# Performance work log

Hardware: AMD Instinct MI355X
Metric: run time of the kernel (lower is better)

## Reference

```python
import jax, jax.numpy as jnp
import numpy as np

N = 32768   # nodes
E = 32768   # edges
ND, ED, GD = 12, 5, 11
H = 64
T = 4
STEPS = 3


def setup_inputs() -> dict:
    key = jax.random.key(0)
    ks = jax.random.split(key, 24)
    s = 0.05
    p = lambda k, sh: (jax.random.normal(k, sh) * s).astype(jnp.float32)
    return dict(
        x=jax.random.normal(ks[0], (N, ND), jnp.float32),
        edge_index=jax.random.randint(ks[1], (2, E), 0, N, jnp.int64),
        edge_attr=jax.random.uniform(ks[2], (E, ED), jnp.float32),
        u=jax.random.normal(ks[3], (1, GD), jnp.float32),
        Wp=p(ks[4], (H, ND + GD)), bp=p(ks[5], (H,)),
        We1=p(ks[6], (H, ED)), be1=p(ks[7], (H,)),
        We2=p(ks[8], (H * H, H)), be2=p(ks[9], (H * H,)),
        root=p(ks[10], (H, H)), conv_b=p(ks[11], (H,)),
        Wih=p(ks[12], (3 * H, H)), bih=p(ks[13], (3 * H,)),
        Whh=p(ks[14], (3 * H, H)), bhh=p(ks[15], (3 * H,)),
        Wd1=p(ks[16], (H, 2 * H + ED)), bd1=p(ks[17], (H,)),
        Wd2=p(ks[18], (H // 2, H)), bd2=p(ks[19], (H // 2,)),
        Wd3=p(ks[20], (T, H // 2)), bd3=p(ks[21], (T,)),
    )


def _forward(x, edge_index, edge_attr, u,
             Wp, bp, We1, be1, We2, be2, root, conv_b,
             Wih, bih, Whh, bhh, Wd1, bd1, Wd2, bd2, Wd3, bd3):
    n = x.shape[0]
    e = edge_attr.shape[0]
    src, dst = edge_index[0], edge_index[1]

    # input projection with broadcast global features (batch=None path)
    u_node = jnp.broadcast_to(u, (n, u.shape[-1]))
    h = jnp.tanh(jnp.concatenate([x, u_node], axis=-1) @ Wp.T + bp)

    # edge MLP -> per-edge (H,H) weight matrices; edge_attr is loop-invariant
    ew = jax.nn.relu(edge_attr @ We1.T + be1) @ We2.T + be2   # (E, H*H)
    ew = ew.reshape(e, H, H)                                   # (E, H, H)

    # mean-aggregation denominators (clamped to 1 like scatter-mean)
    counts = jnp.clip(jax.ops.segment_sum(jnp.ones((e,), h.dtype), dst, num_segments=n), 1.0)

    for _ in range(STEPS):
        # NNConv: gather src features, per-edge matmul, scatter-mean into dst
        msg = jnp.einsum('eh,eho->eo', h[src], ew)             # (E, H)
        agg = jax.ops.segment_sum(msg, dst, num_segments=n) / counts[:, None]
        m = jax.nn.relu(agg + h @ root + conv_b)               # dropout off (eval)
        # GRUCell (torch gate order: r, z, n)
        gi = m @ Wih.T + bih
        gh = h @ Whh.T + bhh
        r = jax.nn.sigmoid(gi[:, :H] + gh[:, :H])
        z = jax.nn.sigmoid(gi[:, H:2 * H] + gh[:, H:2 * H])
        ng = jnp.tanh(gi[:, 2 * H:] + r * gh[:, 2 * H:])
        h = (1.0 - z) * ng + z * h

    # per-edge decoder
    e_in = jnp.concatenate([h[src], h[dst], edge_attr], axis=-1)
    d = jax.nn.relu(e_in @ Wd1.T + bd1)
    d = jax.nn.relu(d @ Wd2.T + bd2)
    return d @ Wd3.T + bd3                                     # (E, T)


def reference(x, edge_index, edge_attr, u,
              Wp, bp, We1, be1, We2, be2, root, conv_b,
              Wih, bih, Whh, bhh, Wd1, bd1, Wd2, bd2, Wd3, bd3):
    return _forward(x, edge_index, edge_attr, u,
                    Wp, bp, We1, be1, We2, be2, root, conv_b,
                    Wih, bih, Whh, bhh, Wd1, bd1, Wd2, bd2, Wd3, bd3)
```

## Files before the change

kernel.cpp:

```cpp
#include <hip/hip_runtime.h>
#include <hip/hip_bf16.h>
#include <stdint.h>


#define N_NODES 32768
#define N_EDGES 32768
#define STEPS 3

typedef __attribute__((ext_vector_type(8))) short short8;
typedef __attribute__((ext_vector_type(4))) float float4v;

__device__ __forceinline__ float bf2f(unsigned short u) {
    union { unsigned int i; float f; } v; v.i = ((unsigned int)u) << 16; return v.f;
}
__device__ __forceinline__ unsigned short f2bf(float f) {
    union { float f; unsigned int i; } v; v.f = f;
    unsigned int x = v.i;
    return (unsigned short)((x + 0x7fffu + ((x >> 16) & 1u)) >> 16);
}

__device__ __forceinline__ void gload_lds16(const void* g, void* l) {
    __builtin_amdgcn_global_load_lds(
        (__attribute__((address_space(1))) void*)g,
        (__attribute__((address_space(3))) void*)l, 16, 0, 0);
}

__global__ __launch_bounds__(256) void k_setup(
    const float* __restrict__ root, const float* __restrict__ Wih,
    const float* __restrict__ Whh,
    const float* __restrict__ We2, const float* __restrict__ be2,
    const float* __restrict__ Wd1, const float* __restrict__ bd1,
    const float* __restrict__ Wd2,
    const float* __restrict__ x, const float* __restrict__ u,
    const float* __restrict__ Wp, const float* __restrict__ bp,
    const float* __restrict__ ea, const float* __restrict__ We1,
    const float* __restrict__ be1,
    unsigned short* __restrict__ rootTf, unsigned short* __restrict__ wcombf,
    unsigned short* __restrict__ w2tf,
    unsigned short* __restrict__ wd1f, unsigned short* __restrict__ wd2f,
    unsigned short* __restrict__ hb,
    unsigned short* __restrict__ hidT, float* __restrict__ cnts)
{
    int b = blockIdx.x, tid = threadIdx.x;
    if (b < 144) {
        int i = b * 256 + tid;
        if (i < 4096) {
            int j = i & 7, lane = (i >> 3) & 63, g = i >> 9;
            int kb = g >> 2, nf = g & 3;
            int o = nf * 16 + (lane & 15);
            int k = kb * 32 + (lane >> 4) * 8 + j;
            rootTf[i] = f2bf(root[k * 64 + o]);
        } else if (i < 4096 + 32768) {
            int t = i - 4096;
            int j = t & 7, lane = (t >> 3) & 63, g = t >> 9;
            int kb = g >> 4, nf = g & 15;
            int cp = nf * 16 + (lane & 15);
            int k = kb * 32 + (lane >> 4) * 8 + j;
            float v;
            if (cp < 128)      v = (k < 64) ? Wih[cp * 64 + k] : Whh[cp * 64 + (k - 64)];
            else if (cp < 192) v = (k < 64) ? Wih[cp * 64 + k] : 0.f;
            else               v = (k < 64) ? 0.f : Whh[(cp - 64) * 64 + (k - 64)];
            wcombf[t] = f2bf(v);
        }
    } else if (b < 1184) {
        int t = (b - 144) * 256 + tid;
        if (t < 65 * 4096) {
            int kk = t >> 12, r = t & 4095;
            int j = r & 7, lane = (r >> 3) & 63, g = r >> 9;
            int half = g >> 2, nf = g & 3;
            int o = nf * 16 + (lane & 15);
            int hh = half * 32 + (lane >> 4) * 8 + j;
            float v = (kk < 64) ? We2[((size_t)(hh * 64 + o)) * 64 + kk]
                                : be2[(size_t)hh * 64 + o];
            w2tf[t] = f2bf(v);
        }
    } else if (b < 1232) {
        int i = (b - 1184) * 256 + tid;
        if (i < 10240) {
            int j = i & 7, lane = (i >> 3) & 63, g = i >> 9;
            int kb = g >> 2, nf = g & 3;
            int o = nf * 16 + (lane & 15);
            int k = kb * 32 + (lane >> 4) * 8 + j;
            float v = (k < 133) ? Wd1[(size_t)o * 133 + k] : (k == 133 ? bd1[o] : 0.f);
            wd1f[i] = f2bf(v);
        } else if (i < 10240 + 2048) {
            int t = i - 10240;
            int j = t & 7, lane = (t >> 3) & 63, g = t >> 9;
            int kb = g >> 1, nf = g & 1;
            int o = nf * 16 + (lane & 15);
            int k = kb * 32 + (lane >> 4) * 8 + j;
            wd2f[t] = f2bf(Wd2[(size_t)o * 64 + k]);
        }
    } else if (b < 9424) {
        int idx = (b - 1232) * 256 + tid;
        int n = idx >> 6, j = idx & 63;
        const float* wr = Wp + j * 23;
        const float* xr = x + (size_t)n * 12;
        float s = bp[j];
#pragma unroll
        for (int i = 0; i < 12; i++) s += xr[i] * wr[i];
#pragma unroll
        for (int i = 0; i < 11; i++) s += u[i] * wr[12 + i];
        hb[idx] = f2bf(tanhf(s));
    } else if (b < 17616) {
        int idx = (b - 9424) * 256 + tid;
        int el = idx & 63, j = (idx >> 6) & 63, eb = idx >> 12;
        int e = eb * 64 + el;
        float s = be1[j];
#pragma unroll
        for (int i = 0; i < 5; i++) s += ea[(size_t)e * 5 + i] * We1[j * 5 + i];
        hidT[(size_t)j * N_EDGES + e] = f2bf(s > 0.f ? s : 0.f);
    } else {
        int idx = (b - 17616) * 1024 + tid * 4;
        if (idx < 32768) {
            float4v z = {0.f, 0.f, 0.f, 0.f};
            *(float4v*)(cnts + idx) = z;
        }
    }
}

__global__ __launch_bounds__(256) void k_counts(
    const int* __restrict__ ei, float* __restrict__ counts)
{
    int i = blockIdx.x * 256 + threadIdx.x;
    if (i < N_EDGES) atomicAdd(&counts[ei[N_EDGES + i]], 1.0f);
}

__global__ __launch_bounds__(1024) void k_scan(
    const float* __restrict__ cnts, int* __restrict__ off, int* __restrict__ woff)
{
    __shared__ int part[1024];
    int t = threadIdx.x;
    int loc[32];
    int s = 0;
#pragma unroll
    for (int i = 0; i < 32; i++) { loc[i] = s; s += (int)cnts[t * 32 + i]; }
    part[t] = s;
    __syncthreads();
    for (int d = 1; d < 1024; d <<= 1) {
        int y = (t >= d) ? part[t - d] : 0;
        __syncthreads();
        part[t] += y;
        __syncthreads();
    }
    int pre = (t == 0) ? 0 : part[t - 1];
#pragma unroll
    for (int i = 0; i < 32; i++) {
        off[t * 32 + i] = pre + loc[i];
        woff[t * 32 + i] = pre + loc[i];
    }
    if (t == 1023) off[32768] = part[1023];
}

__global__ __launch_bounds__(256) void k_scatter(
    const int* __restrict__ ei, int* __restrict__ woff, int* __restrict__ eorder)
{
    int e = blockIdx.x * 256 + threadIdx.x;
    if (e < N_EDGES) {
        int d = ei[N_EDGES + e];
        int slot = atomicAdd(&woff[d], 1);
        eorder[slot] = e;
    }
}

__global__ __launch_bounds__(512, 2) void k_msg_fused(
    const unsigned short* __restrict__ hidT,
    const unsigned short* __restrict__ hb,
    const unsigned short* __restrict__ w2tf,
    const int* __restrict__ ei,
    float* __restrict__ msgbuf)
{
    __shared__ __attribute__((aligned(16))) unsigned char smem[98304];
    unsigned short* stg = (unsigned short*)smem;
    unsigned short* hvl = (unsigned short*)(smem + 65536);
    float* red = (float*)smem;

    int tid = threadIdx.x, w = tid >> 6, lane = tid & 63;
    int l15 = lane & 15, quad = lane >> 4;
    int kg = w & 3, nfh = w >> 2;
    int ebase = blockIdx.x * 128;
    int n_w = 16 + (kg == 3 ? 1 : 0);

    unsigned short* hvp = hvl + w * 2048;
#pragma unroll
    for (int r2 = 0; r2 < 16; r2++) {
        unsigned int v = *((const unsigned int*)(hidT + (size_t)(kg * 16 + r2) * N_EDGES + ebase) + lane);
        *((unsigned int*)hvp + r2 * 64 + lane) = v;
    }
    short8 afr[8][2];
#pragma unroll
    for (int t = 0; t < 8; t++) {
        int src = ei[ebase + t * 16 + l15];
#pragma unroll
        for (int hh = 0; hh < 2; hh++)
            afr[t][hh] = *(const short8*)(hb + (size_t)src * 64 + hh * 32 + quad * 8);
    }

    unsigned short* wbuf = stg + w * 4096;
    auto stage = [&](int r, int db) {
        const unsigned short* g = w2tf + (size_t)(kg * 16 + r) * 4096;
        unsigned short* d = wbuf + db * 2048;
#pragma unroll
        for (int c = 0; c < 4; c++) {
            int hh = c >> 1, j = c & 1;
            gload_lds16(g + (hh * 4 + nfh * 2 + j) * 512 + lane * 8, d + c * 512);
        }
    };

    stage(0, 0);
    stage(1, 1);
    asm volatile("s_waitcnt lgkmcnt(0)" ::: "memory");

    float4v acc[8][2] = {};
    for (int r = 0; r < n_w; r++) {
        int db = r & 1;
        if (r < n_w - 1) { asm volatile("s_waitcnt vmcnt(4)" ::: "memory"); }
        else             { asm volatile("s_waitcnt vmcnt(0)" ::: "memory"); }

        bool bias = (r == 16);
        short8 bfr[2][2];
        const unsigned short* bb = wbuf + db * 2048;
#pragma unroll
        for (int hh = 0; hh < 2; hh++)
#pragma unroll
            for (int j = 0; j < 2; j++)
                bfr[hh][j] = *(const short8*)(bb + (hh * 2 + j) * 512 + lane * 8);

        unsigned long long hu[8] = {};
        if (!bias) {
#pragma unroll
            for (int t = 0; t < 8; t++)
                hu[t] = *(const unsigned long long*)(hvp + r * 128 + t * 16 + quad * 4);
        }

        asm volatile("s_waitcnt lgkmcnt(0)" ::: "memory");
        if (r + 2 < n_w) stage(r + 2, db);

#pragma unroll
        for (int t = 0; t < 8; t++) {
            float4v z = {0.f, 0.f, 0.f, 0.f};
            float4v T0 = __builtin_amdgcn_mfma_f32_16x16x32_bf16(afr[t][0], bfr[0][0], z, 0, 0, 0);
            T0 = __builtin_amdgcn_mfma_f32_16x16x32_bf16(afr[t][1], bfr[1][0], T0, 0, 0, 0);
            float4v T1 = __builtin_amdgcn_mfma_f32_16x16x32_bf16(afr[t][0], bfr[0][1], z, 0, 0, 0);
            T1 = __builtin_amdgcn_mfma_f32_16x16x32_bf16(afr[t][1], bfr[1][1], T1, 0, 0, 0);
#pragma unroll
            for (int rr = 0; rr < 4; rr++) {
                float hvv = bias ? 1.0f : bf2f((unsigned short)(hu[t] >> (16 * rr)));
                acc[t][0][rr] += hvv * T0[rr];
                acc[t][1][rr] += hvv * T1[rr];
            }
        }
    }

    int row_r = tid >> 2, cq = tid & 3;
#pragma unroll
    for (int nf2 = 0; nf2 < 2; nf2++) {
        __syncthreads();
#pragma unroll
        for (int t = 0; t < 8; t++)
#pragma unroll
            for (int rr = 0; rr < 4; rr++)
                red[kg * 4352 + (t * 16 + quad * 4 + rr) * 34 + nfh * 16 + l15] = acc[t][nf2][rr];
        __syncthreads();
        float s[8];
#pragma unroll
        for (int i = 0; i < 8; i++) s[i] = 0.f;
#pragma unroll
        for (int g2 = 0; g2 < 4; g2++) {
            const float* rp = red + g2 * 4352 + row_r * 34 + cq * 8;
#pragma unroll
            for (int i = 0; i < 8; i++) s[i] += rp[i];
        }
        int c34 = cq * 8;
        int gcol = ((c34 >> 4) * 2 + nf2) * 16 + (c34 & 15);
        float* op = msgbuf + (size_t)(ebase + row_r) * 64 + gcol;
        float4v v0 = { s[0], s[1], s[2], s[3] };
        float4v v1 = { s[4], s[5], s[6], s[7] };
        *(float4v*)(op) = v0;
        *(float4v*)(op + 4) = v1;
    }
}

__global__ __launch_bounds__(256) void k_node(
    const unsigned short* __restrict__ hb_in,
    const unsigned short* __restrict__ rootTf,
    const unsigned short* __restrict__ wcombf,
    const float* __restrict__ msgbuf, const int* __restrict__ off,
    const int* __restrict__ eorder,
    const float* __restrict__ counts,
    const float* __restrict__ conv_b,
    const float* __restrict__ bih, const float* __restrict__ bhh,
    unsigned short* __restrict__ hb_out)
{
    __shared__ unsigned short m_lds[64 * 72];
    __shared__ float aggl[64 * 68];
    int tid = threadIdx.x, w = tid >> 6, lane = tid & 63;
    int l15 = lane & 15, quad = lane >> 4;
    int node0 = blockIdx.x * 64;
    int row0 = w * 16;

    {
        int nl = tid >> 2, cg = tid & 3;
        int nn = node0 + nl;
        int s0 = off[nn], s1 = off[nn + 1];
        float acc[16] = {};
        for (int sl = s0; sl < s1; sl++) {
            int e = eorder[sl];
            const float* mr = msgbuf + (size_t)e * 64 + cg * 16;
#pragma unroll
            for (int q = 0; q < 4; q++) {
                float4v v = *(const float4v*)(mr + 4 * q);
#pragma unroll
                for (int j = 0; j < 4; j++) acc[4 * q + j] += v[j];
            }
        }
#pragma unroll
        for (int k = 0; k < 16; k++) aggl[nl * 68 + cg * 16 + k] = acc[k];
    }
    __syncthreads();

    float4v acc1[4] = {};
    {
        short8 a1[2];
#pragma unroll
        for (int kb = 0; kb < 2; kb++)
            a1[kb] = *(const short8*)(hb_in + (size_t)(node0 + row0 + l15) * 64 + kb * 32 + quad * 8);
#pragma unroll
        for (int kb = 0; kb < 2; kb++)
#pragma unroll
            for (int nf = 0; nf < 4; nf++) {
                short8 b = *(const short8*)(rootTf + (size_t)((kb * 4 + nf) * 64 + lane) * 8);
                acc1[nf] = __builtin_amdgcn_mfma_f32_16x16x32_bf16(a1[kb], b, acc1[nf], 0, 0, 0);
            }
    }
#pragma unroll
    for (int rr = 0; rr < 4; rr++) {
        int nl = row0 + quad * 4 + rr;
        float cnt = counts[node0 + nl]; if (cnt < 1.f) cnt = 1.f;
        float rcp = 1.f / cnt;
#pragma unroll
        for (int nf = 0; nf < 4; nf++) {
            int c = nf * 16 + l15;
            float av = aggl[nl * 68 + c];
            float mv = av * rcp + acc1[nf][rr] + conv_b[c];
            m_lds[nl * 72 + c] = f2bf(mv > 0.f ? mv : 0.f);
        }
    }
    __syncthreads();

    float4v acc2[16] = {};
#pragma unroll
    for (int kb = 0; kb < 4; kb++) {
        short8 a2;
        if (kb < 2)
            a2 = *(const short8*)(m_lds + (row0 + l15) * 72 + kb * 32 + quad * 8);
        else
            a2 = *(const short8*)(hb_in + (size_t)(node0 + row0 + l15) * 64 + (kb - 2) * 32 + quad * 8);
#pragma unroll
        for (int nf = 0; nf < 16; nf++) {
            short8 b = *(const short8*)(wcombf + (size_t)((kb * 16 + nf) * 64 + lane) * 8);
            acc2[nf] = __builtin_amdgcn_mfma_f32_16x16x32_bf16(a2, b, acc2[nf], 0, 0, 0);
        }
    }

#pragma unroll
    for (int nf0 = 0; nf0 < 4; nf0++) {
        int c = nf0 * 16 + l15;
        float br = bih[c] + bhh[c];
        float bz = bih[64 + c] + bhh[64 + c];
        float bni = bih[128 + c], bnh = bhh[128 + c];
#pragma unroll
        for (int rr = 0; rr < 4; rr++) {
            int node = node0 + row0 + quad * 4 + rr;
            float gr = 1.f / (1.f + __expf(-(acc2[nf0][rr] + br)));
            float gz = 1.f / (1.f + __expf(-(acc2[nf0 + 4][rr] + bz)));
            float ng = tanhf(acc2[nf0 + 8][rr] + bni + gr * (acc2[nf0 + 12][rr] + bnh));
            float ho = bf2f(hb_in[(size_t)node * 64 + c]);
            float hn = (1.f - gz) * ng + gz * ho;
            hb_out[(size_t)node * 64 + c] = f2bf(hn);
        }
    }
}

__global__ __launch_bounds__(256) void k_decoder(
    const unsigned short* __restrict__ hb, const int* __restrict__ ei,
    const float* __restrict__ ea,
    const unsigned short* __restrict__ wd1f, const unsigned short* __restrict__ wd2f,
    const float* __restrict__ bd2,
    const float* __restrict__ Wd3, const float* __restrict__ bd3,
    float* __restrict__ out)
{
    __shared__ unsigned short d1f[4][1024];
    __shared__ float d2s[4][16 * 33];
    int tid = threadIdx.x, w = tid >> 6, lane = tid & 63;
    int l15 = lane & 15, quad = lane >> 4;
    int ebase = blockIdx.x * 64 + w * 16;
    int e = ebase + l15;
    int src = ei[e], dst = ei[N_EDGES + e];

    short8 a[5];
#pragma unroll
    for (int kb = 0; kb < 2; kb++) {
        a[kb]     = *(const short8*)(hb + (size_t)src * 64 + kb * 32 + quad * 8);
        a[2 + kb] = *(const short8*)(hb + (size_t)dst * 64 + kb * 32 + quad * 8);
    }
    {
        union { short8 v; unsigned short u[8]; } tea;
#pragma unroll
        for (int j = 0; j < 8; j++) {
            float vv = 0.f;
            if (quad == 0) vv = (j < 5) ? ea[(size_t)e * 5 + j] : (j == 5 ? 1.f : 0.f);
            tea.u[j] = f2bf(vv);
        }
        a[4] = tea.v;
    }

    float4v acc1[4] = {};
#pragma unroll
    for (int kb = 0; kb < 5; kb++)
#pragma unroll
        for (int nf = 0; nf < 4; nf++) {
            short8 b = *(const short8*)(wd1f + (size_t)((kb * 4 + nf) * 64 + lane) * 8);
            acc1[nf] = __builtin_amdgcn_mfma_f32_16x16x32_bf16(a[kb], b, acc1[nf], 0, 0, 0);
        }
#pragma unroll
    for (int nf = 0; nf < 4; nf++) {
        int kbp = nf >> 1;
        int lanep_hi = ((nf & 1) * 2 + (l15 >> 3)) * 16;
        int jp = l15 & 7;
#pragma unroll
        for (int r = 0; r < 4; r++) {
            float v = acc1[nf][r];
            d1f[w][kbp * 512 + (lanep_hi + quad * 4 + r) * 8 + jp] = f2bf(v > 0.f ? v : 0.f);
        }
    }
    float4v acc2[2] = {};
#pragma unroll
    for (int kb = 0; kb < 2; kb++) {
        short8 a2 = *(const short8*)(&d1f[w][kb * 512 + lane * 8]);
#pragma unroll
        for (int nf = 0; nf < 2; nf++) {
            short8 b = *(const short8*)(wd2f + (size_t)((kb * 2 + nf) * 64 + lane) * 8);
            acc2[nf] = __builtin_amdgcn_mfma_f32_16x16x32_bf16(a2, b, acc2[nf], 0, 0, 0);
        }
    }
#pragma unroll
    for (int nf = 0; nf < 2; nf++) {
        int c = nf * 16 + l15;
        float bias = bd2[c];
#pragma unroll
        for (int r = 0; r < 4; r++) {
            float v = acc2[nf][r] + bias;
            d2s[w][(quad * 4 + r) * 33 + c] = v > 0.f ? v : 0.f;
        }
    }
    {
        int e_l = lane >> 2, t = lane & 3;
        float s = bd3[t];
        const float* w3 = Wd3 + t * 32;
        const float* dr = &d2s[w][e_l * 33];
#pragma unroll
        for (int k = 0; k < 32; k++) s += w3[k] * dr[k];
        out[(size_t)(ebase + e_l) * 4 + t] = s;
    }
}

extern "C" void kernel_launch(void* const* d_in, const int* in_sizes, int n_in,
                              void* d_out, int out_size, void* d_ws, size_t ws_size,
                              hipStream_t stream)
{
    const float* x      = (const float*)d_in[0];
    const int*   ei     = (const int*)d_in[1];
    const float* ea     = (const float*)d_in[2];
    const float* u      = (const float*)d_in[3];
    const float* Wp     = (const float*)d_in[4];
    const float* bp     = (const float*)d_in[5];
    const float* We1    = (const float*)d_in[6];
    const float* be1    = (const float*)d_in[7];
    const float* We2    = (const float*)d_in[8];
    const float* be2    = (const float*)d_in[9];
    const float* root   = (const float*)d_in[10];
    const float* conv_b = (const float*)d_in[11];
    const float* Wih    = (const float*)d_in[12];
    const float* bih    = (const float*)d_in[13];
    const float* Whh    = (const float*)d_in[14];
    const float* bhh    = (const float*)d_in[15];
    const float* Wd1    = (const float*)d_in[16];
    const float* bd1    = (const float*)d_in[17];
    const float* Wd2    = (const float*)d_in[18];
    const float* bd2    = (const float*)d_in[19];
    const float* Wd3    = (const float*)d_in[20];
    const float* bd3    = (const float*)d_in[21];
    float* out = (float*)d_out;

    char* ws = (char*)d_ws;
    size_t off_b = 0;
    auto take = [&](size_t bytes) -> char* {
        char* p = ws + off_b; off_b = (off_b + bytes + 255) & ~(size_t)255; return p;
    };
    unsigned short* hb     = (unsigned short*)take((size_t)N_NODES * 64 * 2);
    unsigned short* hidT   = (unsigned short*)take((size_t)N_EDGES * 64 * 2);
    float*          msgbuf = (float*)take((size_t)N_EDGES * 64 * 4);
    float*          cnts   = (float*)take((size_t)N_NODES * 4);
    int*            off    = (int*)take((size_t)(N_NODES + 1) * 4);
    int*            woff   = (int*)take((size_t)N_NODES * 4);
    int*            eorder = (int*)take((size_t)N_EDGES * 4);
    unsigned short* w2tf   = (unsigned short*)take((size_t)66 * 4096 * 2);
    unsigned short* rootTf = (unsigned short*)take((size_t)4096 * 2);
    unsigned short* wcombf = (unsigned short*)take((size_t)32768 * 2);
    unsigned short* wd1f   = (unsigned short*)take((size_t)10240 * 2);
    unsigned short* wd2f   = (unsigned short*)take((size_t)2048 * 2);
    (void)ws_size;

    k_setup<<<17648, 256, 0, stream>>>(root, Wih, Whh, We2, be2, Wd1, bd1, Wd2,
                                       x, u, Wp, bp, ea, We1, be1,
                                       rootTf, wcombf, w2tf, wd1f, wd2f,
                                       hb, hidT, cnts);
    k_counts<<<128, 256, 0, stream>>>(ei, cnts);
    k_scan<<<1, 1024, 0, stream>>>(cnts, off, woff);
    k_scatter<<<128, 256, 0, stream>>>(ei, woff, eorder);

    for (int s = 0; s < STEPS; s++) {
        k_msg_fused<<<N_EDGES / 128, 512, 0, stream>>>(hidT, hb, w2tf, ei, msgbuf);
        k_node<<<N_NODES / 64, 256, 0, stream>>>(hb, rootTf, wcombf, msgbuf, off,
                                                 eorder, cnts, conv_b, bih, bhh, hb);
    }
    k_decoder<<<N_EDGES / 64, 256, 0, stream>>>(hb, ei, ea, wd1f, wd2f, bd2,
                                                Wd3, bd3, out);
}
```

Baseline: 261.9 us.

## Fuse message, node-update and decoder kernels into one persistent grid-barrier kernel

Replaces the per-step message and node kernel launches and the final decoder launch with a single persistent kernel of 256 blocks. A software grid barrier (atomic counter plus generation flag) separates the message, aggregation/GRU and decoder phases. Each block now covers 128 edges and 128 nodes, and reuses one shared-memory buffer across phases. This removes the launch gaps and tail effects between the seven kernels. The risks are spin-barrier overhead, and a deadlock if all 256 blocks cannot be resident at once.

```diff
diff --git a/kernel.cpp b/kernel.cpp
--- a/kernel.cpp
+++ b/kernel.cpp
@@ -6,6 +6,7 @@
 #define N_NODES 32768
 #define N_EDGES 32768
 #define STEPS 3
+#define NBLK 256
 
 typedef __attribute__((ext_vector_type(8))) short short8;
 typedef __attribute__((ext_vector_type(4))) float float4v;
@@ -23,6 +24,24 @@
     __builtin_amdgcn_global_load_lds(
         (__attribute__((address_space(1))) void*)g,
         (__attribute__((address_space(3))) void*)l, 16, 0, 0);
+}
+
+__device__ __forceinline__ void grid_barrier(unsigned int* bar) {
+    __syncthreads();
+    if (threadIdx.x == 0) {
+        __threadfence();
+        unsigned g = __hip_atomic_load(&bar[1], __ATOMIC_RELAXED, __HIP_MEMORY_SCOPE_AGENT);
+        unsigned v = __hip_atomic_fetch_add(&bar[0], 1u, __ATOMIC_ACQ_REL, __HIP_MEMORY_SCOPE_AGENT);
+        if (v == (unsigned)(NBLK - 1)) {
+            __hip_atomic_store(&bar[0], 0u, __ATOMIC_RELAXED, __HIP_MEMORY_SCOPE_AGENT);
+            __hip_atomic_store(&bar[1], g + 1u, __ATOMIC_RELEASE, __HIP_MEMORY_SCOPE_AGENT);
+        } else {
+            while (__hip_atomic_load(&bar[1], __ATOMIC_ACQUIRE, __HIP_MEMORY_SCOPE_AGENT) == g)
+                __builtin_amdgcn_s_sleep(8);
+        }
+        __threadfence();
+    }
+    __syncthreads();
 }
 
 __global__ __launch_bounds__(256) void k_setup(
@@ -127,10 +146,12 @@
 }
 
 __global__ __launch_bounds__(1024) void k_scan(
-    const float* __restrict__ cnts, int* __restrict__ off, int* __restrict__ woff)
+    const float* __restrict__ cnts, int* __restrict__ off, int* __restrict__ woff,
+    unsigned int* __restrict__ bar)
 {
     __shared__ int part[1024];
     int t = threadIdx.x;
+    if (t == 0) { bar[0] = 0u; bar[1] = 0u; }
     int loc[32];
     int s = 0;
 #pragma unroll
@@ -163,22 +184,39 @@
     }
 }
 
-__global__ __launch_bounds__(512, 2) void k_msg_fused(
+__global__ __launch_bounds__(512, 2) void k_mega(
     const unsigned short* __restrict__ hidT,
-    const unsigned short* __restrict__ hb,
+    unsigned short* __restrict__ hb,
     const unsigned short* __restrict__ w2tf,
     const int* __restrict__ ei,
-    float* __restrict__ msgbuf)
+    float* __restrict__ msgbuf,
+    const unsigned short* __restrict__ rootTf,
+    const unsigned short* __restrict__ wcombf,
+    const int* __restrict__ off, const int* __restrict__ eorder,
+    const float* __restrict__ cnts, const float* __restrict__ conv_b,
+    const float* __restrict__ bih, const float* __restrict__ bhh,
+    const float* __restrict__ ea,
+    const unsigned short* __restrict__ wd1f, const unsigned short* __restrict__ wd2f,
+    const float* __restrict__ bd2,
+    const float* __restrict__ Wd3, const float* __restrict__ bd3,
+    float* __restrict__ out,
+    unsigned int* __restrict__ bar)
 {
-    __shared__ __attribute__((aligned(16))) unsigned char smem[98304];
-    unsigned short* stg = (unsigned short*)smem;
-    unsigned short* hvl = (unsigned short*)(smem + 65536);
-    float* red = (float*)smem;
+    __shared__ __attribute__((aligned(16))) unsigned char smem[102400];
+    unsigned short* stg   = (unsigned short*)smem;
+    unsigned short* hvl   = (unsigned short*)(smem + 69632);
+    float*          red   = (float*)smem;
+    unsigned short* m_lds = (unsigned short*)smem;
+    float*          aggl  = (float*)(smem + 18432);
+    unsigned short* d1f   = (unsigned short*)smem;
+    float*          d2s   = (float*)(smem + 16384);
 
     int tid = threadIdx.x, w = tid >> 6, lane = tid & 63;
     int l15 = lane & 15, quad = lane >> 4;
+    int bid = blockIdx.x;
     int kg = w & 3, nfh = w >> 2;
-    int ebase = blockIdx.x * 128;
+    int ebase = bid * 128;
+    int node0 = bid * 128;
     int n_w = 16 + (kg == 3 ? 1 : 0);
 
     unsigned short* hvp = hvl + w * 2048;
@@ -186,14 +224,6 @@
     for (int r2 = 0; r2 < 16; r2++) {
         unsigned int v = *((const unsigned int*)(hidT + (size_t)(kg * 16 + r2) * N_EDGES + ebase) + lane);
         *((unsigned int*)hvp + r2 * 64 + lane) = v;
-    }
-    short8 afr[8][2];
-#pragma unroll
-    for (int t = 0; t < 8; t++) {
-        int src = ei[ebase + t * 16 + l15];
-#pragma unroll
-        for (int hh = 0; hh < 2; hh++)
-            afr[t][hh] = *(const short8*)(hb + (size_t)src * 64 + hh * 32 + quad * 8);
     }
 
     unsigned short* wbuf = stg + w * 4096;
@@ -207,261 +237,246 @@
         }
     };
 
-    stage(0, 0);
-    stage(1, 1);
-    asm volatile("s_waitcnt lgkmcnt(0)" ::: "memory");
-
-    float4v acc[8][2] = {};
-    for (int r = 0; r < n_w; r++) {
-        int db = r & 1;
-        if (r < n_w - 1) { asm volatile("s_waitcnt vmcnt(4)" ::: "memory"); }
-        else             { asm volatile("s_waitcnt vmcnt(0)" ::: "memory"); }
-
-        bool bias = (r == 16);
-        short8 bfr[2][2];
-        const unsigned short* bb = wbuf + db * 2048;
-#pragma unroll
-        for (int hh = 0; hh < 2; hh++)
-#pragma unroll
-            for (int j = 0; j < 2; j++)
-                bfr[hh][j] = *(const short8*)(bb + (hh * 2 + j) * 512 + lane * 8);
-
-        unsigned long long hu[8] = {};
-        if (!bias) {
+    for (int step = 0; step < STEPS; step++) {
+        short8 afr[8][2];
+#pragma unroll
+        for (int t = 0; t < 8; t++) {
+            int src = ei[ebase + t * 16 + l15];
+#pragma unroll
+            for (int hh = 0; hh < 2; hh++)
+                afr[t][hh] = *(const short8*)(hb + (size_t)src * 64 + hh * 32 + quad * 8);
+        }
+        stage(0, 0);
+        stage(1, 1);
+        asm volatile("s_waitcnt lgkmcnt(0)" ::: "memory");
+
+        float4v acc[8][2] = {};
+        for (int r = 0; r < n_w; r++) {
+            int db = r & 1;
+            if (r < n_w - 1) { asm volatile("s_waitcnt vmcnt(4)" ::: "memory"); }
+            else             { asm volatile("s_waitcnt vmcnt(0)" ::: "memory"); }
+
+            bool bias = (r == 16);
+            short8 bfr[2][2];
+            const unsigned short* bb = wbuf + db * 2048;
+#pragma unroll
+            for (int hh = 0; hh < 2; hh++)
+#pragma unroll
+                for (int j = 0; j < 2; j++)
+                    bfr[hh][j] = *(const short8*)(bb + (hh * 2 + j) * 512 + lane * 8);
+
+            unsigned long long hu[8] = {};
+            if (!bias) {
+#pragma unroll
+                for (int t = 0; t < 8; t++)
+                    hu[t] = *(const unsigned long long*)(hvp + r * 128 + t * 16 + quad * 4);
+            }
+
+            asm volatile("s_waitcnt lgkmcnt(0)" ::: "memory");
+            if (r + 2 < n_w) stage(r + 2, db);
+
+#pragma unroll
+            for (int t = 0; t < 8; t++) {
+                float4v z = {0.f, 0.f, 0.f, 0.f};
+                float4v T0 = __builtin_amdgcn_mfma_f32_16x16x32_bf16(afr[t][0], bfr[0][0], z, 0, 0, 0);
+                T0 = __builtin_amdgcn_mfma_f32_16x16x32_bf16(afr[t][1], bfr[1][0], T0, 0, 0, 0);
+                float4v T1 = __builtin_amdgcn_mfma_f32_16x16x32_bf16(afr[t][0], bfr[0][1], z, 0, 0, 0);
+                T1 = __builtin_amdgcn_mfma_f32_16x16x32_bf16(afr[t][1], bfr[1][1], T1, 0, 0, 0);
+#pragma unroll
+                for (int rr = 0; rr < 4; rr++) {
+                    float hvv = bias ? 1.0f : bf2f((unsigned short)(hu[t] >> (16 * rr)));
+                    acc[t][0][rr] += hvv * T0[rr];
+                    acc[t][1][rr] += hvv * T1[rr];
+                }
+            }
+        }
+
+        int row_r = tid >> 2, cq = tid & 3;
+#pragma unroll
+        for (int nf2 = 0; nf2 < 2; nf2++) {
+            __syncthreads();
 #pragma unroll
             for (int t = 0; t < 8; t++)
-                hu[t] = *(const unsigned long long*)(hvp + r * 128 + t * 16 + quad * 4);
-        }
-
-        asm volatile("s_waitcnt lgkmcnt(0)" ::: "memory");
-        if (r + 2 < n_w) stage(r + 2, db);
-
-#pragma unroll
-        for (int t = 0; t < 8; t++) {
-            float4v z = {0.f, 0.f, 0.f, 0.f};
-            float4v T0 = __builtin_amdgcn_mfma_f32_16x16x32_bf16(afr[t][0], bfr[0][0], z, 0, 0, 0);
-            T0 = __builtin_amdgcn_mfma_f32_16x16x32_bf16(afr[t][1], bfr[1][0], T0, 0, 0, 0);
-            float4v T1 = __builtin_amdgcn_mfma_f32_16x16x32_bf16(afr[t][0], bfr[0][1], z, 0, 0, 0);
-            T1 = __builtin_amdgcn_mfma_f32_16x16x32_bf16(afr[t][1], bfr[1][1], T1, 0, 0, 0);
+#pragma unroll
+                for (int rr = 0; rr < 4; rr++)
+                    red[kg * 4352 + (t * 16 + quad * 4 + rr) * 34 + nfh * 16 + l15] = acc[t][nf2][rr];
+            __syncthreads();
+            float s[8];
+#pragma unroll
+            for (int i = 0; i < 8; i++) s[i] = 0.f;
+#pragma unroll
+            for (int g2 = 0; g2 < 4; g2++) {
+                const float* rp = red + g2 * 4352 + row_r * 34 + cq * 8;
+#pragma unroll
+                for (int i = 0; i < 8; i++) s[i] += rp[i];
+            }
+            int c34 = cq * 8;
+            int gcol = ((c34 >> 4) * 2 + nf2) * 16 + (c34 & 15);
+            float* op = msgbuf + (size_t)(ebase + row_r) * 64 + gcol;
+            float4v v0 = { s[0], s[1], s[2], s[3] };
+            float4v v1 = { s[4], s[5], s[6], s[7] };
+            *(float4v*)(op) = v0;
+            *(float4v*)(op + 4) = v1;
+        }
+
+        grid_barrier(bar);
+
+        {
+            int nl = tid >> 2, cg = tid & 3;
+            int nn = node0 + nl;
+            int s0 = off[nn], s1 = off[nn + 1];
+            float accg[16] = {};
+            for (int sl = s0; sl < s1; sl++) {
+                int e = eorder[sl];
+                const float* mr = msgbuf + (size_t)e * 64 + cg * 16;
+#pragma unroll
+                for (int q = 0; q < 4; q++) {
+                    float4v v = *(const float4v*)(mr + 4 * q);
+#pragma unroll
+                    for (int j = 0; j < 4; j++) accg[4 * q + j] += v[j];
+                }
+            }
+#pragma unroll
+            for (int k = 0; k < 16; k++) aggl[nl * 68 + cg * 16 + k] = accg[k];
+        }
+        __syncthreads();
+
+        int row0 = w * 16;
+        float4v acc1[4] = {};
+        {
+            short8 a1[2];
+#pragma unroll
+            for (int kb = 0; kb < 2; kb++)
+                a1[kb] = *(const short8*)(hb + (size_t)(node0 + row0 + l15) * 64 + kb * 32 + quad * 8);
+#pragma unroll
+            for (int kb = 0; kb < 2; kb++)
+#pragma unroll
+                for (int nf = 0; nf < 4; nf++) {
+                    short8 b = *(const short8*)(rootTf + (size_t)((kb * 4 + nf) * 64 + lane) * 8);
+                    acc1[nf] = __builtin_amdgcn_mfma_f32_16x16x32_bf16(a1[kb], b, acc1[nf], 0, 0, 0);
+                }
+        }
+#pragma unroll
+        for (int rr = 0; rr < 4; rr++) {
+            int nl = row0 + quad * 4 + rr;
+            float cnt = cnts[node0 + nl]; if (cnt < 1.f) cnt = 1.f;
+            float rcp = 1.f / cnt;
+#pragma unroll
+            for (int nf = 0; nf < 4; nf++) {
+                int c = nf * 16 + l15;
+                float av = aggl[nl * 68 + c];
+                float mv = av * rcp + acc1[nf][rr] + conv_b[c];
+                m_lds[nl * 72 + c] = f2bf(mv > 0.f ? mv : 0.f);
+            }
+        }
+        __syncthreads();
+
+        float4v acc2[16] = {};
+#pragma unroll
+        for (int kb = 0; kb < 4; kb++) {
+            short8 a2;
+            if (kb < 2)
+                a2 = *(const short8*)(m_lds + (row0 + l15) * 72 + kb * 32 + quad * 8);
+            else
+                a2 = *(const short8*)(hb + (size_t)(node0 + row0 + l15) * 64 + (kb - 2) * 32 + quad * 8);
+#pragma unroll
+            for (int nf = 0; nf < 16; nf++) {
+                short8 b = *(const short8*)(wcombf + (size_t)((kb * 16 + nf) * 64 + lane) * 8);
+                acc2[nf] = __builtin_amdgcn_mfma_f32_16x16x32_bf16(a2, b, acc2[nf], 0, 0, 0);
+            }
+        }
+
+#pragma unroll
+        for (int nf0 = 0; nf0 < 4; nf0++) {
+            int c = nf0 * 16 + l15;
+            float br = bih[c] + bhh[c];
+            float bz = bih[64 + c] + bhh[64 + c];
+            float bni = bih[128 + c], bnh = bhh[128 + c];
 #pragma unroll
             for (int rr = 0; rr < 4; rr++) {
-                float hvv = bias ? 1.0f : bf2f((unsigned short)(hu[t] >> (16 * rr)));
-                acc[t][0][rr] += hvv * T0[rr];
-                acc[t][1][rr] += hvv * T1[rr];
-            }
-        }
-    }
-
-    int row_r = tid >> 2, cq = tid & 3;
-#pragma unroll
-    for (int nf2 = 0; nf2 < 2; nf2++) {
-        __syncthreads();
-#pragma unroll
-        for (int t = 0; t < 8; t++)
-#pragma unroll
-            for (int rr = 0; rr < 4; rr++)
-                red[kg * 4352 + (t * 16 + quad * 4 + rr) * 34 + nfh * 16 + l15] = acc[t][nf2][rr];
-        __syncthreads();
-        float s[8];
-#pragma unroll
-        for (int i = 0; i < 8; i++) s[i] = 0.f;
-#pragma unroll
-        for (int g2 = 0; g2 < 4; g2++) {
-            const float* rp = red + g2 * 4352 + row_r * 34 + cq * 8;
-#pragma unroll
-            for (int i = 0; i < 8; i++) s[i] += rp[i];
-        }
-        int c34 = cq * 8;
-        int gcol = ((c34 >> 4) * 2 + nf2) * 16 + (c34 & 15);
-        float* op = msgbuf + (size_t)(ebase + row_r) * 64 + gcol;
-        float4v v0 = { s[0], s[1], s[2], s[3] };
-        float4v v1 = { s[4], s[5], s[6], s[7] };
-        *(float4v*)(op) = v0;
-        *(float4v*)(op + 4) = v1;
-    }
-}
-
-__global__ __launch_bounds__(256) void k_node(
-    const unsigned short* __restrict__ hb_in,
-    const unsigned short* __restrict__ rootTf,
-    const unsigned short* __restrict__ wcombf,
-    const float* __restrict__ msgbuf, const int* __restrict__ off,
-    const int* __restrict__ eorder,
-    const float* __restrict__ counts,
-    const float* __restrict__ conv_b,
-    const float* __restrict__ bih, const float* __restrict__ bhh,
-    unsigned short* __restrict__ hb_out)
-{
-    __shared__ unsigned short m_lds[64 * 72];
-    __shared__ float aggl[64 * 68];
-    int tid = threadIdx.x, w = tid >> 6, lane = tid & 63;
-    int l15 = lane & 15, quad = lane >> 4;
-    int node0 = blockIdx.x * 64;
-    int row0 = w * 16;
+                int node = node0 + row0 + quad * 4 + rr;
+                float gr = 1.f / (1.f + __expf(-(acc2[nf0][rr] + br)));
+                float gz = 1.f / (1.f + __expf(-(acc2[nf0 + 4][rr] + bz)));
+                float ng = tanhf(acc2[nf0 + 8][rr] + bni + gr * (acc2[nf0 + 12][rr] + bnh));
+                float ho = bf2f(hb[(size_t)node * 64 + c]);
+                float hn = (1.f - gz) * ng + gz * ho;
+                hb[(size_t)node * 64 + c] = f2bf(hn);
+            }
+        }
+
+        grid_barrier(bar);
+    }
 
     {
-        int nl = tid >> 2, cg = tid & 3;
-        int nn = node0 + nl;
-        int s0 = off[nn], s1 = off[nn + 1];
-        float acc[16] = {};
-        for (int sl = s0; sl < s1; sl++) {
-            int e = eorder[sl];
-            const float* mr = msgbuf + (size_t)e * 64 + cg * 16;
-#pragma unroll
-            for (int q = 0; q < 4; q++) {
-                float4v v = *(const float4v*)(mr + 4 * q);
-#pragma unroll
-                for (int j = 0; j < 4; j++) acc[4 * q + j] += v[j];
-            }
-        }
-#pragma unroll
-        for (int k = 0; k < 16; k++) aggl[nl * 68 + cg * 16 + k] = acc[k];
-    }
-    __syncthreads();
-
-    float4v acc1[4] = {};
-    {
-        short8 a1[2];
-#pragma unroll
-        for (int kb = 0; kb < 2; kb++)
-            a1[kb] = *(const short8*)(hb_in + (size_t)(node0 + row0 + l15) * 64 + kb * 32 + quad * 8);
-#pragma unroll
-        for (int kb = 0; kb < 2; kb++)
+        int eb_d = bid * 128 + w * 16;
+        int e = eb_d + l15;
+        int src = ei[e], dst = ei[N_EDGES + e];
+
+        short8 a[5];
+#pragma unroll
+        for (int kb = 0; kb < 2; kb++) {
+            a[kb]     = *(const short8*)(hb + (size_t)src * 64 + kb * 32 + quad * 8);
+            a[2 + kb] = *(const short8*)(hb + (size_t)dst * 64 + kb * 32 + quad * 8);
+        }
+        {
+            union { short8 v; unsigned short u[8]; } tea;
+#pragma unroll
+            for (int j = 0; j < 8; j++) {
+                float vv = 0.f;
+                if (quad == 0) vv = (j < 5) ? ea[(size_t)e * 5 + j] : (j == 5 ? 1.f : 0.f);
+                tea.u[j] = f2bf(vv);
+            }
+            a[4] = tea.v;
+        }
+
+        float4v acc1[4] = {};
+#pragma unroll
+        for (int kb = 0; kb < 5; kb++)
 #pragma unroll
             for (int nf = 0; nf < 4; nf++) {
-                short8 b = *(const short8*)(rootTf + (size_t)((kb * 4 + nf) * 64 + lane) * 8);
-                acc1[nf] = __builtin_amdgcn_mfma_f32_16x16x32_bf16(a1[kb], b, acc1[nf], 0, 0, 0);
-            }
-    }
-#pragma unroll
-    for (int rr = 0; rr < 4; rr++) {
-        int nl = row0 + quad * 4 + rr;
-        float cnt = counts[node0 + nl]; if (cnt < 1.f) cnt = 1.f;
-        float rcp = 1.f / cnt;
+                short8 b = *(const short8*)(wd1f + (size_t)((kb * 4 + nf) * 64 + lane) * 8);
+                acc1[nf] = __builtin_amdgcn_mfma_f32_16x16x32_bf16(a[kb], b, acc1[nf], 0, 0, 0);
+            }
 #pragma unroll
         for (int nf = 0; nf < 4; nf++) {
+            int kbp = nf >> 1;
+            int lanep_hi = ((nf & 1) * 2 + (l15 >> 3)) * 16;
+            int jp = l15 & 7;
+#pragma unroll
+            for (int r = 0; r < 4; r++) {
+                float v = acc1[nf][r];
+                d1f[w * 1024 + kbp * 512 + (lanep_hi + quad * 4 + r) * 8 + jp] = f2bf(v > 0.f ? v : 0.f);
+            }
+        }
+        float4v acc2[2] = {};
+#pragma unroll
+        for (int kb = 0; kb < 2; kb++) {
+            short8 a2 = *(const short8*)(&d1f[w * 1024 + kb * 512 + lane * 8]);
+#pragma unroll
+            for (int nf = 0; nf < 2; nf++) {
+                short8 b = *(const short8*)(wd2f + (size_t)((kb * 2 + nf) * 64 + lane) * 8);
+                acc2[nf] = __builtin_amdgcn_mfma_f32_16x16x32_bf16(a2, b, acc2[nf], 0, 0, 0);
+            }
+        }
+#pragma unroll
+        for (int nf = 0; nf < 2; nf++) {
             int c = nf * 16 + l15;
-            float av = aggl[nl * 68 + c];
-            float mv = av * rcp + acc1[nf][rr] + conv_b[c];
-            m_lds[nl * 72 + c] = f2bf(mv > 0.f ? mv : 0.f);
-        }
-    }
-    __syncthreads();
-
-    float4v acc2[16] = {};
-#pragma unroll
-    for (int kb = 0; kb < 4; kb++) {
-        short8 a2;
-        if (kb < 2)
-            a2 = *(const short8*)(m_lds + (row0 + l15) * 72 + kb * 32 + quad * 8);
-        else
-            a2 = *(const short8*)(hb_in + (size_t)(node0 + row0 + l15) * 64 + (kb - 2) * 32 + quad * 8);
-#pragma unroll
-        for (int nf = 0; nf < 16; nf++) {
-            short8 b = *(const short8*)(wcombf + (size_t)((kb * 16 + nf) * 64 + lane) * 8);
-            acc2[nf] = __builtin_amdgcn_mfma_f32_16x16x32_bf16(a2, b, acc2[nf], 0, 0, 0);
-        }
-    }
-
-#pragma unroll
-    for (int nf0 = 0; nf0 < 4; nf0++) {
-        int c = nf0 * 16 + l15;
-        float br = bih[c] + bhh[c];
-        float bz = bih[64 + c] + bhh[64 + c];
-        float bni = bih[128 + c], bnh = bhh[128 + c];
-#pragma unroll
-        for (int rr = 0; rr < 4; rr++) {
-            int node = node0 + row0 + quad * 4 + rr;
-            float gr = 1.f / (1.f + __expf(-(acc2[nf0][rr] + br)));
-            float gz = 1.f / (1.f + __expf(-(acc2[nf0 + 4][rr] + bz)));
-            float ng = tanhf(acc2[nf0 + 8][rr] + bni + gr * (acc2[nf0 + 12][rr] + bnh));
-            float ho = bf2f(hb_in[(size_t)node * 64 + c]);
-            float hn = (1.f - gz) * ng + gz * ho;
-            hb_out[(size_t)node * 64 + c] = f2bf(hn);
-        }
-    }
-}
-
-__global__ __launch_bounds__(256) void k_decoder(
-    const unsigned short* __restrict__ hb, const int* __restrict__ ei,
-    const float* __restrict__ ea,
-    const unsigned short* __restrict__ wd1f, const unsigned short* __restrict__ wd2f,
-    const float* __restrict__ bd2,
-    const float* __restrict__ Wd3, const float* __restrict__ bd3,
-    float* __restrict__ out)
-{
-    __shared__ unsigned short d1f[4][1024];
-    __shared__ float d2s[4][16 * 33];
-    int tid = threadIdx.x, w = tid >> 6, lane = tid & 63;
-    int l15 = lane & 15, quad = lane >> 4;
-    int ebase = blockIdx.x * 64 + w * 16;
-    int e = ebase + l15;
-    int src = ei[e], dst = ei[N_EDGES + e];
-
-    short8 a[5];
-#pragma unroll
-    for (int kb = 0; kb < 2; kb++) {
-        a[kb]     = *(const short8*)(hb + (size_t)src * 64 + kb * 32 + quad * 8);
-        a[2 + kb] = *(const short8*)(hb + (size_t)dst * 64 + kb * 32 + quad * 8);
-    }
-    {
-        union { short8 v; unsigned short u[8]; } tea;
-#pragma unroll
-        for (int j = 0; j < 8; j++) {
-            float vv = 0.f;
-            if (quad == 0) vv = (j < 5) ? ea[(size_t)e * 5 + j] : (j == 5 ? 1.f : 0.f);
-            tea.u[j] = f2bf(vv);
-        }
-        a[4] = tea.v;
-    }
-
-    float4v acc1[4] = {};
-#pragma unroll
-    for (int kb = 0; kb < 5; kb++)
-#pragma unroll
-        for (int nf = 0; nf < 4; nf++) {
-            short8 b = *(const short8*)(wd1f + (size_t)((kb * 4 + nf) * 64 + lane) * 8);
-            acc1[nf] = __builtin_amdgcn_mfma_f32_16x16x32_bf16(a[kb], b, acc1[nf], 0, 0, 0);
-        }
-#pragma unroll
-    for (int nf = 0; nf < 4; nf++) {
-        int kbp = nf >> 1;
-        int lanep_hi = ((nf & 1) * 2 + (l15 >> 3)) * 16;
-        int jp = l15 & 7;
-#pragma unroll
-        for (int r = 0; r < 4; r++) {
-            float v = acc1[nf][r];
-            d1f[w][kbp * 512 + (lanep_hi + quad * 4 + r) * 8 + jp] = f2bf(v > 0.f ? v : 0.f);
-        }
-    }
-    float4v acc2[2] = {};
-#pragma unroll
-    for (int kb = 0; kb < 2; kb++) {
-        short8 a2 = *(const short8*)(&d1f[w][kb * 512 + lane * 8]);
-#pragma unroll
-        for (int nf = 0; nf < 2; nf++) {
-            short8 b = *(const short8*)(wd2f + (size_t)((kb * 2 + nf) * 64 + lane) * 8);
-            acc2[nf] = __builtin_amdgcn_mfma_f32_16x16x32_bf16(a2, b, acc2[nf], 0, 0, 0);
-        }
-    }
-#pragma unroll
-    for (int nf = 0; nf < 2; nf++) {
-        int c = nf * 16 + l15;
-        float bias = bd2[c];
-#pragma unroll
-        for (int r = 0; r < 4; r++) {
-            float v = acc2[nf][r] + bias;
-            d2s[w][(quad * 4 + r) * 33 + c] = v > 0.f ? v : 0.f;
-        }
-    }
-    {
-        int e_l = lane >> 2, t = lane & 3;
-        float s = bd3[t];
-        const float* w3 = Wd3 + t * 32;
-        const float* dr = &d2s[w][e_l * 33];
-#pragma unroll
-        for (int k = 0; k < 32; k++) s += w3[k] * dr[k];
-        out[(size_t)(ebase + e_l) * 4 + t] = s;
+            float bias = bd2[c];
+#pragma unroll
+            for (int r = 0; r < 4; r++) {
+                float v = acc2[nf][r] + bias;
+                d2s[w * 528 + (quad * 4 + r) * 33 + c] = v > 0.f ? v : 0.f;
+            }
+        }
+        {
+            int e_l = lane >> 2, t = lane & 3;
+            float s = bd3[t];
+            const float* w3 = Wd3 + t * 32;
+            const float* dr = &d2s[w * 528 + e_l * 33];
+#pragma unroll
+            for (int k = 0; k < 32; k++) s += w3[k] * dr[k];
+            out[(size_t)(eb_d + e_l) * 4 + t] = s;
+        }
     }
 }
 
@@ -505,6 +520,7 @@
     int*            off    = (int*)take((size_t)(N_NODES + 1) * 4);
     int*            woff   = (int*)take((size_t)N_NODES * 4);
     int*            eorder = (int*)take((size_t)N_EDGES * 4);
+    unsigned int*   bar    = (unsigned int*)take(256);
     unsigned short* w2tf   = (unsigned short*)take((size_t)66 * 4096 * 2);
     unsigned short* rootTf = (unsigned short*)take((size_t)4096 * 2);
     unsigned short* wcombf = (unsigned short*)take((size_t)32768 * 2);
@@ -517,14 +533,11 @@
                                        rootTf, wcombf, w2tf, wd1f, wd2f,
                                        hb, hidT, cnts);
     k_counts<<<128, 256, 0, stream>>>(ei, cnts);
-    k_scan<<<1, 1024, 0, stream>>>(cnts, off, woff);
+    k_scan<<<1, 1024, 0, stream>>>(cnts, off, woff, bar);
     k_scatter<<<128, 256, 0, stream>>>(ei, woff, eorder);
 
-    for (int s = 0; s < STEPS; s++) {
-        k_msg_fused<<<N_EDGES / 128, 512, 0, stream>>>(hidT, hb, w2tf, ei, msgbuf);
-        k_node<<<N_NODES / 64, 256, 0, stream>>>(hb, rootTf, wcombf, msgbuf, off,
-                                                 eorder, cnts, conv_b, bih, bhh, hb);
-    }
-    k_decoder<<<N_EDGES / 64, 256, 0, stream>>>(hb, ei, ea, wd1f, wd2f, bd2,
-                                                Wd3, bd3, out);
-}
+    k_mega<<<NBLK, 512, 0, stream>>>(hidT, hb, w2tf, ei, msgbuf,
+                                     rootTf, wcombf, off, eorder, cnts,
+                                     conv_b, bih, bhh, ea, wd1f, wd2f,
+                                     bd2, Wd3, bd3, out, bar);
+}
```

After: 611.4 us. +133.4%, slower.

## Fuse graph CSR build into one LDS kernel and halve msg tile per block

Applied to the files above, without the earlier changes.

Replaces the counts/scan/scatter kernels with a single 1024-thread kernel that counts in-degree with LDS atomics, scans, and fills the edge order, removing two launches and the global atomics. The fused message kernel now handles 64 edges per block instead of 128, using 72KB of LDS and fewer accumulator registers, and targets 4 blocks per CU for higher occupancy. The cost is that each block re-streams the whole edge-weight matrix for half as many edges, doubling weight traffic, and the single-block graph build runs serially on one CU.

```diff
diff --git a/kernel.cpp b/kernel.cpp
--- a/kernel.cpp
+++ b/kernel.cpp
@@ -39,7 +39,7 @@
     unsigned short* __restrict__ w2tf,
     unsigned short* __restrict__ wd1f, unsigned short* __restrict__ wd2f,
     unsigned short* __restrict__ hb,
-    unsigned short* __restrict__ hidT, float* __restrict__ cnts)
+    unsigned short* __restrict__ hidT)
 {
     int b = blockIdx.x, tid = threadIdx.x;
     if (b < 144) {
@@ -102,7 +102,7 @@
 #pragma unroll
         for (int i = 0; i < 11; i++) s += u[i] * wr[12 + i];
         hb[idx] = f2bf(tanhf(s));
-    } else if (b < 17616) {
+    } else {
         int idx = (b - 9424) * 256 + tid;
         int el = idx & 63, j = (idx >> 6) & 63, eb = idx >> 12;
         int e = eb * 64 + el;
@@ -110,31 +110,28 @@
 #pragma unroll
         for (int i = 0; i < 5; i++) s += ea[(size_t)e * 5 + i] * We1[j * 5 + i];
         hidT[(size_t)j * N_EDGES + e] = f2bf(s > 0.f ? s : 0.f);
-    } else {
-        int idx = (b - 17616) * 1024 + tid * 4;
-        if (idx < 32768) {
-            float4v z = {0.f, 0.f, 0.f, 0.f};
-            *(float4v*)(cnts + idx) = z;
-        }
-    }
-}
-
-__global__ __launch_bounds__(256) void k_counts(
-    const int* __restrict__ ei, float* __restrict__ counts)
+    }
+}
+
+__global__ __launch_bounds__(1024) void k_graph(
+    const int* __restrict__ ei, int* __restrict__ off,
+    float* __restrict__ cnts, int* __restrict__ eorder)
 {
-    int i = blockIdx.x * 256 + threadIdx.x;
-    if (i < N_EDGES) atomicAdd(&counts[ei[N_EDGES + i]], 1.0f);
-}
-
-__global__ __launch_bounds__(1024) void k_scan(
-    const float* __restrict__ cnts, int* __restrict__ off, int* __restrict__ woff)
-{
+    __shared__ int cnt[N_NODES];
     __shared__ int part[1024];
     int t = threadIdx.x;
-    int loc[32];
-    int s = 0;
-#pragma unroll
-    for (int i = 0; i < 32; i++) { loc[i] = s; s += (int)cnts[t * 32 + i]; }
+#pragma unroll
+    for (int i = 0; i < 32; i++) cnt[t + i * 1024] = 0;
+    __syncthreads();
+#pragma unroll
+    for (int i = 0; i < 32; i++) {
+        int e = t + i * 1024;
+        atomicAdd(&cnt[ei[N_EDGES + e]], 1);
+    }
+    __syncthreads();
+    int loc[32]; int s = 0;
+#pragma unroll
+    for (int i = 0; i < 32; i++) { loc[i] = s; s += cnt[t * 32 + i]; }
     part[t] = s;
     __syncthreads();
     for (int d = 1; d < 1024; d <<= 1) {
@@ -144,33 +141,36 @@
         __syncthreads();
     }
     int pre = (t == 0) ? 0 : part[t - 1];
+    int base[32];
 #pragma unroll
     for (int i = 0; i < 32; i++) {
-        off[t * 32 + i] = pre + loc[i];
-        woff[t * 32 + i] = pre + loc[i];
-    }
-    if (t == 1023) off[32768] = part[1023];
-}
-
-__global__ __launch_bounds__(256) void k_scatter(
-    const int* __restrict__ ei, int* __restrict__ woff, int* __restrict__ eorder)
-{
-    int e = blockIdx.x * 256 + threadIdx.x;
-    if (e < N_EDGES) {
+        int n = t * 32 + i;
+        base[i] = pre + loc[i];
+        off[n] = base[i];
+        cnts[n] = (float)cnt[n];
+    }
+    if (t == 1023) off[N_NODES] = N_EDGES;
+    __syncthreads();
+#pragma unroll
+    for (int i = 0; i < 32; i++) cnt[t * 32 + i] = base[i];
+    __syncthreads();
+#pragma unroll
+    for (int i = 0; i < 32; i++) {
+        int e = t + i * 1024;
         int d = ei[N_EDGES + e];
-        int slot = atomicAdd(&woff[d], 1);
+        int slot = atomicAdd(&cnt[d], 1);
         eorder[slot] = e;
     }
 }
 
-__global__ __launch_bounds__(512, 2) void k_msg_fused(
+__global__ __launch_bounds__(512, 4) void k_msg_fused(
     const unsigned short* __restrict__ hidT,
     const unsigned short* __restrict__ hb,
     const unsigned short* __restrict__ w2tf,
     const int* __restrict__ ei,
     float* __restrict__ msgbuf)
 {
-    __shared__ __attribute__((aligned(16))) unsigned char smem[98304];
+    __shared__ __attribute__((aligned(16))) unsigned char smem[73728];
     unsigned short* stg = (unsigned short*)smem;
     unsigned short* hvl = (unsigned short*)(smem + 65536);
     float* red = (float*)smem;
@@ -178,18 +178,19 @@
     int tid = threadIdx.x, w = tid >> 6, lane = tid & 63;
     int l15 = lane & 15, quad = lane >> 4;
     int kg = w & 3, nfh = w >> 2;
-    int ebase = blockIdx.x * 128;
+    int ebase = blockIdx.x * 64;
     int n_w = 16 + (kg == 3 ? 1 : 0);
 
-    unsigned short* hvp = hvl + w * 2048;
-#pragma unroll
-    for (int r2 = 0; r2 < 16; r2++) {
-        unsigned int v = *((const unsigned int*)(hidT + (size_t)(kg * 16 + r2) * N_EDGES + ebase) + lane);
-        *((unsigned int*)hvp + r2 * 64 + lane) = v;
-    }
-    short8 afr[8][2];
-#pragma unroll
-    for (int t = 0; t < 8; t++) {
+#pragma unroll
+    for (int i = 0; i < 8; i++) {
+        int row = w * 8 + i;
+        hvl[row * 64 + lane] = hidT[(size_t)row * N_EDGES + ebase + lane];
+    }
+    __syncthreads();
+
+    short8 afr[4][2];
+#pragma unroll
+    for (int t = 0; t < 4; t++) {
         int src = ei[ebase + t * 16 + l15];
 #pragma unroll
         for (int hh = 0; hh < 2; hh++)
@@ -209,9 +210,8 @@
 
     stage(0, 0);
     stage(1, 1);
-    asm volatile("s_waitcnt lgkmcnt(0)" ::: "memory");
-
-    float4v acc[8][2] = {};
+
+    float4v acc[4][2] = {};
     for (int r = 0; r < n_w; r++) {
         int db = r & 1;
         if (r < n_w - 1) { asm volatile("s_waitcnt vmcnt(4)" ::: "memory"); }
@@ -226,58 +226,55 @@
             for (int j = 0; j < 2; j++)
                 bfr[hh][j] = *(const short8*)(bb + (hh * 2 + j) * 512 + lane * 8);
 
-        unsigned long long hu[8] = {};
+        unsigned long long hu[4] = {};
         if (!bias) {
 #pragma unroll
-            for (int t = 0; t < 8; t++)
-                hu[t] = *(const unsigned long long*)(hvp + r * 128 + t * 16 + quad * 4);
+            for (int t = 0; t < 4; t++)
+                hu[t] = *(const unsigned long long*)(hvl + (kg * 16 + r) * 64 + t * 16 + quad * 4);
         }
 
         asm volatile("s_waitcnt lgkmcnt(0)" ::: "memory");
         if (r + 2 < n_w) stage(r + 2, db);
 
 #pragma unroll
-        for (int t = 0; t < 8; t++) {
+        for (int t = 0; t < 4; t++) {
             float4v z = {0.f, 0.f, 0.f, 0.f};
             float4v T0 = __builtin_amdgcn_mfma_f32_16x16x32_bf16(afr[t][0], bfr[0][0], z, 0, 0, 0);
             T0 = __builtin_amdgcn_mfma_f32_16x16x32_bf16(afr[t][1], bfr[1][0], T0, 0, 0, 0);
             float4v T1 = __builtin_amdgcn_mfma_f32_16x16x32_bf16(afr[t][0], bfr[0][1], z, 0, 0, 0);
             T1 = __builtin_amdgcn_mfma_f32_16x16x32_bf16(afr[t][1], bfr[1][1], T1, 0, 0, 0);
-#pragma unroll
-            for (int rr = 0; rr < 4; rr++) {
-                float hvv = bias ? 1.0f : bf2f((unsigned short)(hu[t] >> (16 * rr)));
-                acc[t][0][rr] += hvv * T0[rr];
-                acc[t][1][rr] += hvv * T1[rr];
+            float4v hv4;
+            if (bias) { hv4[0] = hv4[1] = hv4[2] = hv4[3] = 1.0f; }
+            else {
+#pragma unroll
+                for (int rr = 0; rr < 4; rr++)
+                    hv4[rr] = bf2f((unsigned short)(hu[t] >> (16 * rr)));
             }
-        }
-    }
-
-    int row_r = tid >> 2, cq = tid & 3;
+            acc[t][0] += hv4 * T0;
+            acc[t][1] += hv4 * T1;
+        }
+    }
+
+    int row_r = tid >> 3, cq = tid & 7;
 #pragma unroll
     for (int nf2 = 0; nf2 < 2; nf2++) {
         __syncthreads();
 #pragma unroll
-        for (int t = 0; t < 8; t++)
+        for (int t = 0; t < 4; t++)
 #pragma unroll
             for (int rr = 0; rr < 4; rr++)
-                red[kg * 4352 + (t * 16 + quad * 4 + rr) * 34 + nfh * 16 + l15] = acc[t][nf2][rr];
+                red[kg * 2176 + (t * 16 + quad * 4 + rr) * 34 + nfh * 16 + l15] = acc[t][nf2][rr];
         __syncthreads();
-        float s[8];
-#pragma unroll
-        for (int i = 0; i < 8; i++) s[i] = 0.f;
+        float4v s = {0.f, 0.f, 0.f, 0.f};
 #pragma unroll
         for (int g2 = 0; g2 < 4; g2++) {
-            const float* rp = red + g2 * 4352 + row_r * 34 + cq * 8;
-#pragma unroll
-            for (int i = 0; i < 8; i++) s[i] += rp[i];
-        }
-        int c34 = cq * 8;
+            const float* rp = red + g2 * 2176 + row_r * 34 + cq * 4;
+#pragma unroll
+            for (int j = 0; j < 4; j++) s[j] += rp[j];
+        }
+        int c34 = cq * 4;
         int gcol = ((c34 >> 4) * 2 + nf2) * 16 + (c34 & 15);
-        float* op = msgbuf + (size_t)(ebase + row_r) * 64 + gcol;
-        float4v v0 = { s[0], s[1], s[2], s[3] };
-        float4v v1 = { s[4], s[5], s[6], s[7] };
-        *(float4v*)(op) = v0;
-        *(float4v*)(op + 4) = v1;
+        *(float4v*)(msgbuf + (size_t)(ebase + row_r) * 64 + gcol) = s;
     }
 }
 
@@ -503,7 +500,6 @@
     float*          msgbuf = (float*)take((size_t)N_EDGES * 64 * 4);
     float*          cnts   = (float*)take((size_t)N_NODES * 4);
     int*            off    = (int*)take((size_t)(N_NODES + 1) * 4);
-    int*            woff   = (int*)take((size_t)N_NODES * 4);
     int*            eorder = (int*)take((size_t)N_EDGES * 4);
     unsigned short* w2tf   = (unsigned short*)take((size_t)66 * 4096 * 2);
     unsigned short* rootTf = (unsigned short*)take((size_t)4096 * 2);
@@ -512,16 +508,14 @@
     unsigned short* wd2f   = (unsigned short*)take((size_t)2048 * 2);
     (void)ws_size;
 
-    k_setup<<<17648, 256, 0, stream>>>(root, Wih, Whh, We2, be2, Wd1, bd1, Wd2,
+    k_setup<<<17616, 256, 0, stream>>>(root, Wih, Whh, We2, be2, Wd1, bd1, Wd2,
                                        x, u, Wp, bp, ea, We1, be1,
                                        rootTf, wcombf, w2tf, wd1f, wd2f,
-                                       hb, hidT, cnts);
-    k_counts<<<128, 256, 0, stream>>>(ei, cnts);
-    k_scan<<<1, 1024, 0, stream>>>(cnts, off, woff);
-    k_scatter<<<128, 256, 0, stream>>>(ei, woff, eorder);
+                                       hb, hidT);
+    k_graph<<<1, 1024, 0, stream>>>(ei, off, cnts, eorder);
 
     for (int s = 0; s < STEPS; s++) {
-        k_msg_fused<<<N_EDGES / 128, 512, 0, stream>>>(hidT, hb, w2tf, ei, msgbuf);
+        k_msg_fused<<<N_EDGES / 64, 512, 0, stream>>>(hidT, hb, w2tf, ei, msgbuf);
         k_node<<<N_NODES / 64, 256, 0, stream>>>(hb, rootTf, wcombf, msgbuf, off,
                                                  eorder, cnts, conv_b, bih, bhh, hb);
     }
```

After: 313.1 us. 19.5% more time.
